# Kernel tuning notes

Measured on AMD Instinct MI355X. Metric: run time of the kernel, lower is better.

Reference implementation:

```python
import jax, jax.numpy as jnp
import numpy as np

HEADS = 8
DIM_HEAD = 64
SCALE = DIM_HEAD ** -0.5


def setup_inputs() -> dict:
    key = jax.random.key(0)
    k1, k2, k3 = jax.random.split(key, 3)
    B, N, D = 4, 2048, 512
    inner = HEADS * DIM_HEAD  # 512
    x = jax.random.normal(k1, (B, N, D), dtype=jnp.float32)
    # nn.Linear stores weight [out, in]; y = x @ W.T
    w_qkv = jax.random.normal(k2, (3 * inner, D), dtype=jnp.float32) * (D ** -0.5)
    w_out = jax.random.normal(k3, (D, inner), dtype=jnp.float32) * (inner ** -0.5)
    b_out = jnp.zeros((D,), dtype=jnp.float32)
    return {"x": x, "w_qkv": w_qkv, "w_out": w_out, "b_out": b_out}


def reference(x, w_qkv, w_out, b_out):
    B, N, D = x.shape
    qkv = jnp.einsum('bnd,ed->bne', x, w_qkv)  # [B,N,3*inner]
    q, k, v = jnp.split(qkv, 3, axis=-1)
    def to_heads(t):
        return t.reshape(B, N, HEADS, DIM_HEAD).transpose(0, 2, 1, 3)  # [B,H,N,Dh]
    q, k, v = to_heads(q), to_heads(k), to_heads(v)
    dots = jnp.einsum('bhid,bhjd->bhij', q, k) * SCALE  # [B,H,N,N]
    attn = jax.nn.softmax(dots, axis=-1)
    out = jnp.einsum('bhij,bhjd->bhid', attn, v)  # [B,H,N,Dh]
    out = out.transpose(0, 2, 1, 3).reshape(B, N, HEADS * DIM_HEAD)
    return jnp.einsum('bne,de->bnd', out, w_out) + b_out
```

## Files before the change

### kernel.cpp

```cpp
#include <hip/hip_runtime.h>
#include <hip/hip_bf16.h>
#include <stdint.h>

typedef __bf16 bf16;
typedef __bf16 bf16x8 __attribute__((ext_vector_type(8)));
typedef __bf16 bf16x4 __attribute__((ext_vector_type(4)));
typedef float f32x4 __attribute__((ext_vector_type(4)));

template <int V> struct Int { static constexpr int value = V; };

static __device__ __forceinline__ void gl2lds16(const void* g, void* l) {
  const __attribute__((address_space(1))) void* gp =
      reinterpret_cast<const __attribute__((address_space(1))) void*>(
          reinterpret_cast<uintptr_t>(g));
  __attribute__((address_space(3))) void* lp =
      reinterpret_cast<__attribute__((address_space(3))) void*>(
          static_cast<uint32_t>(reinterpret_cast<uintptr_t>(l)));
  __builtin_amdgcn_global_load_lds(gp, lp, 16, 0, 0);
}

static __device__ __forceinline__ float fast_exp2(float x) {
#if __has_builtin(__builtin_amdgcn_exp2f)
  return __builtin_amdgcn_exp2f(x);
#else
  return exp2f(x);
#endif
}

__global__ __launch_bounds__(256) void cvt_all(const float* __restrict__ x,
                                               const float* __restrict__ wq,
                                               const float* __restrict__ wo,
                                               bf16* __restrict__ dst) {
  int i = blockIdx.x * 256 + threadIdx.x;
  const int stride = gridDim.x * 256;
  for (; i < 1310720; i += stride) {
    const float4 v = (i < 1048576) ? reinterpret_cast<const float4*>(x)[i]
                   : (i < 1245184) ? reinterpret_cast<const float4*>(wq)[i - 1048576]
                                   : reinterpret_cast<const float4*>(wo)[i - 1245184];
    bf16x4 o;
    o[0] = (bf16)v.x; o[1] = (bf16)v.y; o[2] = (bf16)v.z; o[3] = (bf16)v.w;
    reinterpret_cast<bf16x4*>(dst)[i] = o;
  }
}

__global__ __launch_bounds__(256) void qkv_gemm(const bf16* __restrict__ X,
                                                const bf16* __restrict__ W,
                                                bf16* __restrict__ Qb,
                                                bf16* __restrict__ Kb,
                                                bf16* __restrict__ Vt) {
  __shared__ __align__(16) bf16 AshX[8192];
  __shared__ __align__(16) bf16 BshX[8192];
  const int t = threadIdx.x;
  const int lane = t & 63;
  const int w = t >> 6;
  const int fr = lane & 15, fg = lane >> 4;
  const int wr = w >> 1, wc = w & 1;
  const int m0 = blockIdx.x * 128;
  const int n0 = blockIdx.y * 128;
  const int r0 = t >> 2, seg = t & 3;
  const bf16* pA0 = X + (m0 + r0) * 512 + seg * 8;
  const bf16* pA1 = X + (m0 + r0 + 64) * 512 + seg * 8;
  const bf16* pB0 = W + (n0 + r0) * 512 + seg * 8;
  const bf16* pB1 = W + (n0 + r0 + 64) * 512 + seg * 8;
  const bf16* ap = AshX + (wr * 64 + fr) * 32 + fg * 8;
  const bf16* bp = BshX + (wc * 64 + fr) * 32 + fg * 8;

  f32x4 acc[4][4] = {};

  auto stage = [&](auto Bt) {
    constexpr int B = decltype(Bt)::value;
    gl2lds16(pA0, (void*)(AshX + B * 4096 + t * 8));
    gl2lds16(pA1, (void*)(AshX + B * 4096 + 2048 + t * 8));
    gl2lds16(pB0, (void*)(BshX + B * 4096 + t * 8));
    gl2lds16(pB1, (void*)(BshX + B * 4096 + 2048 + t * 8));
    pA0 += 32; pA1 += 32; pB0 += 32; pB1 += 32;
  };
  auto step = [&](auto Bt) {
    constexpr int B = decltype(Bt)::value;
    bf16x8 a[4], b[4];
#pragma unroll
    for (int m = 0; m < 4; ++m) a[m] = *reinterpret_cast<const bf16x8*>(ap + B * 4096 + m * 512);
#pragma unroll
    for (int n = 0; n < 4; ++n) b[n] = *reinterpret_cast<const bf16x8*>(bp + B * 4096 + n * 512);
#pragma unroll
    for (int m = 0; m < 4; ++m)
#pragma unroll
      for (int n = 0; n < 4; ++n)
        acc[m][n] = __builtin_amdgcn_mfma_f32_16x16x32_bf16(a[m], b[n], acc[m][n], 0, 0, 0);
  };

  stage(Int<0>{});
  __syncthreads();
  for (int kt = 0; kt < 16; kt += 2) {
    stage(Int<1>{});
    step(Int<0>{});
    __syncthreads();
    if (kt < 14) stage(Int<0>{});
    step(Int<1>{});
    __syncthreads();
  }

  const int which = n0 >> 9;
#pragma unroll
  for (int n = 0; n < 4; ++n) {
    const int e = n0 + wc * 64 + 16 * n + fr;
    const int h = (e >> 6) & 7;
    const int d = e & 63;
#pragma unroll
    for (int m = 0; m < 4; ++m) {
      const int mbase = m0 + wr * 64 + 16 * m + fg * 4;
      if (which == 2) {
        bf16x4 pk;
#pragma unroll
        for (int r = 0; r < 4; ++r) pk[r] = (bf16)acc[m][n][r];
        const int b = mbase >> 11, tok = mbase & 2047;
        *reinterpret_cast<bf16x4*>(&Vt[((b * 8 + h) * 64 + d) * 2048 + tok]) = pk;
      } else {
        bf16* dst = (which == 0) ? Qb : Kb;
        const float sc = (which == 0) ? (0.125f * 1.44269504088896f) : 1.0f;
#pragma unroll
        for (int r = 0; r < 4; ++r) {
          const int row = mbase + r;
          const int b = row >> 11, tok = row & 2047;
          dst[((b * 8 + h) * 2048 + tok) * 64 + d] = (bf16)(acc[m][n][r] * sc);
        }
      }
    }
  }
}

__global__ __launch_bounds__(256, 2) void attn_fwd(const bf16* __restrict__ Qb,
                                                   const bf16* __restrict__ Kb,
                                                   const bf16* __restrict__ Vt,
                                                   bf16* __restrict__ Ob) {
  __shared__ __align__(16) bf16 sh[32768];
  const int t = threadIdx.x;
  const int lane = t & 63;
  const int w = t >> 6;
  const int fr = lane & 15, fg = lane >> 4;
  const int bh = blockIdx.x;
  const int q0 = blockIdx.y * 64 + 16 * w;

  const bf16* Qrow = Qb + (bh * 2048 + q0 + fr) * 64;
  const bf16x8 qf0 = *reinterpret_cast<const bf16x8*>(Qrow + fg * 8);
  const bf16x8 qf1 = *reinterpret_cast<const bf16x8*>(Qrow + 32 + fg * 8);

  bf16x8 ones;
#pragma unroll
  for (int i = 0; i < 8; ++i) ones[i] = (bf16)1.0f;

  const int c0row = t >> 3, cseg = t & 7;
  const int c1row = c0row + 32;
  const int s0 = (cseg ^ (c0row & 7)) * 8;
  const int s1 = (cseg ^ (c1row & 7)) * 8;
  const int kp0 = 32 * ((c0row >> 4) >> 1) + 8 * ((c0row & 15) >> 2) +
                  4 * ((c0row >> 4) & 1) + (c0row & 3);
  const int kp1 = 32 * ((c1row >> 4) >> 1) + 8 * ((c1row & 15) >> 2) +
                  4 * ((c1row >> 4) & 1) + (c1row & 3);
  const bf16* pK0 = Kb + bh * 131072 + kp0 * 64 + s0;
  const bf16* pK1 = Kb + bh * 131072 + kp1 * 64 + s1;
  const bf16* pV0 = Vt + bh * 131072 + c0row * 2048 + s0;
  const bf16* pV1 = Vt + bh * 131072 + c1row * 2048 + s1;

  const int swz = (fr & 7) << 4;
  const int ko0 = fr * 128 + ((fg * 16) ^ swz);
  const int ko1 = fr * 128 + ((64 + fg * 16) ^ swz);
  const char* shb = reinterpret_cast<const char*>(sh);

  f32x4 oacc[4] = {};
  f32x4 lacc = {};
  const f32x4 fzero = {0.f, 0.f, 0.f, 0.f};

  auto stage = [&](auto St) {
    constexpr int S = decltype(St)::value;
    gl2lds16(pK0, (void*)(sh + S * 4096 + t * 8));
    gl2lds16(pK1, (void*)(sh + S * 4096 + 2048 + t * 8));
    gl2lds16(pV0, (void*)(sh + 16384 + S * 4096 + t * 8));
    gl2lds16(pV1, (void*)(sh + 16384 + S * 4096 + 2048 + t * 8));
    pK0 += 4096; pK1 += 4096; pV0 += 64; pV1 += 64;
  };

  auto compute = [&](auto St) {
    constexpr int S = decltype(St)::value;
    f32x4 s[4];
#pragma unroll
    for (int j = 0; j < 4; ++j) {
      const bf16x8 kf0 = *reinterpret_cast<const bf16x8*>(shb + ko0 + (S * 8192 + j * 2048));
      s[j] = __builtin_amdgcn_mfma_f32_16x16x32_bf16(kf0, qf0, fzero, 0, 0, 0);
      const bf16x8 kf1 = *reinterpret_cast<const bf16x8*>(shb + ko1 + (S * 8192 + j * 2048));
      s[j] = __builtin_amdgcn_mfma_f32_16x16x32_bf16(kf1, qf1, s[j], 0, 0, 0);
    }
    bf16x8 pf[2];
#pragma unroll
    for (int j = 0; j < 4; ++j)
#pragma unroll
      for (int r = 0; r < 4; ++r) {
        pf[j >> 1][4 * (j & 1) + r] = (bf16)fast_exp2(s[j][r]);
      }
    __builtin_amdgcn_s_setprio(1);
#pragma unroll
    for (int ss = 0; ss < 2; ++ss) {
      lacc = __builtin_amdgcn_mfma_f32_16x16x32_bf16(ones, pf[ss], lacc, 0, 0, 0);
#pragma unroll
      for (int j = 0; j < 4; ++j) {
        const bf16x8 vf = *reinterpret_cast<const bf16x8*>(
            shb + (ss ? ko1 : ko0) + (32768 + S * 8192 + j * 2048));
        oacc[j] = __builtin_amdgcn_mfma_f32_16x16x32_bf16(vf, pf[ss], oacc[j], 0, 0, 0);
      }
    }
    __builtin_amdgcn_s_setprio(0);
  };

  auto phase = [&](auto ReadS, auto StageS, auto Vm) {
    constexpr int ST = decltype(StageS)::value;
    constexpr int VM = decltype(Vm)::value;
    if constexpr (ST >= 0) stage(Int<ST>{});
    if constexpr (VM == 8) asm volatile("s_waitcnt vmcnt(8)" ::: "memory");
    else if constexpr (VM == 4) asm volatile("s_waitcnt vmcnt(4)" ::: "memory");
    else asm volatile("s_waitcnt vmcnt(0)" ::: "memory");
    __builtin_amdgcn_s_barrier();
    __builtin_amdgcn_sched_barrier(0);
    compute(ReadS);
  };

  stage(Int<0>{});
  stage(Int<1>{});
  for (int kt = 0; kt < 28; kt += 4) {
    phase(Int<0>{}, Int<2>{}, Int<8>{});
    phase(Int<1>{}, Int<3>{}, Int<8>{});
    phase(Int<2>{}, Int<0>{}, Int<8>{});
    phase(Int<3>{}, Int<1>{}, Int<8>{});
  }
  phase(Int<0>{}, Int<2>{}, Int<8>{});
  phase(Int<1>{}, Int<3>{}, Int<8>{});
  phase(Int<2>{}, Int<-1>{}, Int<4>{});
  phase(Int<3>{}, Int<-1>{}, Int<0>{});

  const int b = bh >> 3, h = bh & 7;
  const int q = q0 + fr;
  const float inv = 1.0f / lacc[0];
#pragma unroll
  for (int j = 0; j < 4; ++j) {
    bf16x4 o4;
#pragma unroll
    for (int r = 0; r < 4; ++r) o4[r] = (bf16)(oacc[j][r] * inv);
    *reinterpret_cast<bf16x4*>(&Ob[(b * 2048 + q) * 512 + h * 64 + 16 * j + 4 * fg]) = o4;
  }
}

__global__ __launch_bounds__(256) void out_gemm(const bf16* __restrict__ O,
                                                const bf16* __restrict__ W,
                                                const float* __restrict__ bias,
                                                float* __restrict__ Y) {
  __shared__ __align__(16) bf16 Ash[2][64 * 32];
  __shared__ __align__(16) bf16 Bsh[2][64 * 32];
  const int t = threadIdx.x;
  const int lane = t & 63;
  const int w = t >> 6;
  const int fr = lane & 15, fg = lane >> 4;
  const int m0 = blockIdx.x * 64;
  const int n0 = blockIdx.y * 64;
  const int srow = t >> 2, sseg = t & 3;
  const bf16* gA = O + (m0 + srow) * 512 + sseg * 8;
  const bf16* gB = W + (n0 + srow) * 512 + sseg * 8;

  f32x4 acc[4] = {};
  gl2lds16(gA, &Ash[0][t * 8]);
  gl2lds16(gB, &Bsh[0][t * 8]);
  __syncthreads();
  int cur = 0;
  for (int kt = 0; kt < 16; ++kt) {
    if (kt < 15) {
      gl2lds16(gA + (kt + 1) * 32, &Ash[cur ^ 1][t * 8]);
      gl2lds16(gB + (kt + 1) * 32, &Bsh[cur ^ 1][t * 8]);
    }
    const bf16x8 a = *reinterpret_cast<const bf16x8*>(&Ash[cur][(16 * w + fr) * 32 + fg * 8]);
#pragma unroll
    for (int j = 0; j < 4; ++j) {
      const bf16x8 b = *reinterpret_cast<const bf16x8*>(&Bsh[cur][(16 * j + fr) * 32 + fg * 8]);
      acc[j] = __builtin_amdgcn_mfma_f32_16x16x32_bf16(a, b, acc[j], 0, 0, 0);
    }
    __syncthreads();
    cur ^= 1;
  }
  const int mbase = m0 + 16 * w + fg * 4;
#pragma unroll
  for (int j = 0; j < 4; ++j) {
    const int col = n0 + 16 * j + fr;
    const float bv = bias[col];
#pragma unroll
    for (int r = 0; r < 4; ++r) {
      Y[(mbase + r) * 512 + col] = acc[j][r] + bv;
    }
  }
}

extern "C" void kernel_launch(void* const* d_in, const int* in_sizes, int n_in,
                              void* d_out, int out_size, void* d_ws, size_t ws_size,
                              hipStream_t stream) {
  const float* x = (const float*)d_in[0];
  const float* w_qkv = (const float*)d_in[1];
  const float* w_out = (const float*)d_in[2];
  const float* b_out = (const float*)d_in[3];
  float* y = (float*)d_out;
  char* ws = (char*)d_ws;
  bf16* xb    = (bf16*)(ws);
  bf16* wqkvb = (bf16*)(ws + 8388608);
  bf16* woutb = (bf16*)(ws + 9961472);
  bf16* Qb    = (bf16*)(ws + 10485760);
  bf16* Kb    = (bf16*)(ws + 18874368);
  bf16* Vt    = (bf16*)(ws + 27262976);
  bf16* Ob    = (bf16*)(ws + 35651584);

  hipLaunchKernelGGL(cvt_all, dim3(5120), dim3(256), 0, stream, x, w_qkv, w_out, xb);
  hipLaunchKernelGGL(qkv_gemm, dim3(64, 12), dim3(256), 0, stream, xb, wqkvb, Qb, Kb, Vt);
  hipLaunchKernelGGL(attn_fwd, dim3(32, 32), dim3(256), 0, stream, Qb, Kb, Vt, Ob);
  hipLaunchKernelGGL(out_gemm, dim3(128, 8), dim3(256), 0, stream, Ob, woutb, b_out, y);
}
```

Baseline: 82.29 us.

## Halve attention LDS buffering to double occupancy with a two-stage pipeline

The attention kernel drops from four K/V LDS stages to two, halving shared memory use, and raises the launch bound from 2 to 4 blocks per CU. The hand-tuned vmcnt-based phase schedule is replaced by a simple double-buffered loop synchronized with __syncthreads. The exp2 work for the second half of each tile is also split off so it can overlap with the first half's P·V MFMAs. In exchange, prefetch depth is shorter and each barrier now waits for all outstanding loads, which can expose more memory latency per wave; the added occupancy is meant to hide it.

```diff
diff --git a/kernel.cpp b/kernel.cpp
--- a/kernel.cpp
+++ b/kernel.cpp
@@ -129,11 +129,11 @@
   }
 }
 
-__global__ __launch_bounds__(256, 2) void attn_fwd(const bf16* __restrict__ Qb,
+__global__ __launch_bounds__(256, 4) void attn_fwd(const bf16* __restrict__ Qb,
                                                    const bf16* __restrict__ Kb,
                                                    const bf16* __restrict__ Vt,
                                                    bf16* __restrict__ Ob) {
-  __shared__ __align__(16) bf16 sh[32768];
+  __shared__ __align__(16) bf16 sh[16384];
   const int t = threadIdx.x;
   const int lane = t & 63;
   const int w = t >> 6;
@@ -175,8 +175,8 @@
     constexpr int S = decltype(St)::value;
     gl2lds16(pK0, (void*)(sh + S * 4096 + t * 8));
     gl2lds16(pK1, (void*)(sh + S * 4096 + 2048 + t * 8));
-    gl2lds16(pV0, (void*)(sh + 16384 + S * 4096 + t * 8));
-    gl2lds16(pV1, (void*)(sh + 16384 + S * 4096 + 2048 + t * 8));
+    gl2lds16(pV0, (void*)(sh + 8192 + S * 4096 + t * 8));
+    gl2lds16(pV1, (void*)(sh + 8192 + S * 4096 + 2048 + t * 8));
     pK0 += 4096; pK1 += 4096; pV0 += 64; pV1 += 64;
   };
 
@@ -190,51 +190,46 @@
       const bf16x8 kf1 = *reinterpret_cast<const bf16x8*>(shb + ko1 + (S * 8192 + j * 2048));
       s[j] = __builtin_amdgcn_mfma_f32_16x16x32_bf16(kf1, qf1, s[j], 0, 0, 0);
     }
-    bf16x8 pf[2];
-#pragma unroll
-    for (int j = 0; j < 4; ++j)
-#pragma unroll
-      for (int r = 0; r < 4; ++r) {
-        pf[j >> 1][4 * (j & 1) + r] = (bf16)fast_exp2(s[j][r]);
-      }
+    bf16x8 pf0;
+#pragma unroll
+    for (int j = 0; j < 2; ++j)
+#pragma unroll
+      for (int r = 0; r < 4; ++r) pf0[4 * j + r] = (bf16)fast_exp2(s[j][r]);
     __builtin_amdgcn_s_setprio(1);
-#pragma unroll
-    for (int ss = 0; ss < 2; ++ss) {
-      lacc = __builtin_amdgcn_mfma_f32_16x16x32_bf16(ones, pf[ss], lacc, 0, 0, 0);
-#pragma unroll
-      for (int j = 0; j < 4; ++j) {
-        const bf16x8 vf = *reinterpret_cast<const bf16x8*>(
-            shb + (ss ? ko1 : ko0) + (32768 + S * 8192 + j * 2048));
-        oacc[j] = __builtin_amdgcn_mfma_f32_16x16x32_bf16(vf, pf[ss], oacc[j], 0, 0, 0);
-      }
+    lacc = __builtin_amdgcn_mfma_f32_16x16x32_bf16(ones, pf0, lacc, 0, 0, 0);
+#pragma unroll
+    for (int j = 0; j < 4; ++j) {
+      const bf16x8 vf = *reinterpret_cast<const bf16x8*>(
+          shb + ko0 + (16384 + S * 8192 + j * 2048));
+      oacc[j] = __builtin_amdgcn_mfma_f32_16x16x32_bf16(vf, pf0, oacc[j], 0, 0, 0);
+    }
+    __builtin_amdgcn_s_setprio(0);
+    bf16x8 pf1;
+#pragma unroll
+    for (int j = 2; j < 4; ++j)
+#pragma unroll
+      for (int r = 0; r < 4; ++r) pf1[4 * (j - 2) + r] = (bf16)fast_exp2(s[j][r]);
+    __builtin_amdgcn_s_setprio(1);
+    lacc = __builtin_amdgcn_mfma_f32_16x16x32_bf16(ones, pf1, lacc, 0, 0, 0);
+#pragma unroll
+    for (int j = 0; j < 4; ++j) {
+      const bf16x8 vf = *reinterpret_cast<const bf16x8*>(
+          shb + ko1 + (16384 + S * 8192 + j * 2048));
+      oacc[j] = __builtin_amdgcn_mfma_f32_16x16x32_bf16(vf, pf1, oacc[j], 0, 0, 0);
     }
     __builtin_amdgcn_s_setprio(0);
   };
 
-  auto phase = [&](auto ReadS, auto StageS, auto Vm) {
-    constexpr int ST = decltype(StageS)::value;
-    constexpr int VM = decltype(Vm)::value;
-    if constexpr (ST >= 0) stage(Int<ST>{});
-    if constexpr (VM == 8) asm volatile("s_waitcnt vmcnt(8)" ::: "memory");
-    else if constexpr (VM == 4) asm volatile("s_waitcnt vmcnt(4)" ::: "memory");
-    else asm volatile("s_waitcnt vmcnt(0)" ::: "memory");
-    __builtin_amdgcn_s_barrier();
-    __builtin_amdgcn_sched_barrier(0);
-    compute(ReadS);
-  };
-
   stage(Int<0>{});
-  stage(Int<1>{});
-  for (int kt = 0; kt < 28; kt += 4) {
-    phase(Int<0>{}, Int<2>{}, Int<8>{});
-    phase(Int<1>{}, Int<3>{}, Int<8>{});
-    phase(Int<2>{}, Int<0>{}, Int<8>{});
-    phase(Int<3>{}, Int<1>{}, Int<8>{});
-  }
-  phase(Int<0>{}, Int<2>{}, Int<8>{});
-  phase(Int<1>{}, Int<3>{}, Int<8>{});
-  phase(Int<2>{}, Int<-1>{}, Int<4>{});
-  phase(Int<3>{}, Int<-1>{}, Int<0>{});
+  __syncthreads();
+  for (int kt = 0; kt < 32; kt += 2) {
+    stage(Int<1>{});
+    compute(Int<0>{});
+    __syncthreads();
+    if (kt < 30) stage(Int<0>{});
+    compute(Int<1>{});
+    __syncthreads();
+  }
 
   const int b = bh >> 3, h = bh & 7;
   const int q = q0 + fr;
```

Result: no change. 83.75 us (+1.8%).
